# Performance work log

Hardware: AMD Instinct MI355X
Metric: run time of the kernel (lower is better)

The kernel has to match this reference:

```python
import jax, jax.numpy as jnp
import numpy as np

DIM, E, K, H = 1024, 8, 2, 4096

def setup_inputs() -> dict:
    key = jax.random.key(0)
    ks = jax.random.split(key, 5)
    s_in = 1.0 / np.sqrt(DIM)
    s_h = 1.0 / np.sqrt(H)
    return {
        "x": jax.random.normal(ks[0], (4, 2048, DIM), dtype=jnp.float32),
        "Wr": jax.random.normal(ks[1], (DIM, E), dtype=jnp.float32) * s_in,
        "W1": jax.random.normal(ks[2], (E, DIM, H), dtype=jnp.float32) * s_in,
        "b1": jnp.zeros((E, H), dtype=jnp.float32),
        "W2": jax.random.normal(ks[3], (E, H, DIM), dtype=jnp.float32) * s_h,
        "b2": jnp.zeros((E, DIM), dtype=jnp.float32),
    }

def reference(x, Wr, W1, b1, W2, b2):
    batch, seq, dim = x.shape
    x_flat = x.reshape(-1, dim)                      # [T, D]
    logits = x_flat @ Wr                             # [T, E]
    w, ind = jax.lax.top_k(logits, K)                # [T, K]
    w = jax.nn.softmax(w, axis=-1)
    # combine[t, e] = sum_i w[t, i] * (ind[t, i] == e)
    combine = jnp.einsum('tke,tk->te', jax.nn.one_hot(ind, E, dtype=x.dtype), w)  # [T, E]

    def body(acc, params):
        W1e, b1e, W2e, b2e, ce = params
        h = jax.nn.gelu(x_flat @ W1e + b1e, approximate=False)  # exact GELU (torch nn.GELU default)
        y = h @ W2e + b2e                                        # [T, D]
        return acc + ce[:, None] * y, None

    out0 = jnp.zeros_like(x_flat)
    out, _ = jax.lax.scan(body, out0, (W1, b1, W2, b2, combine.T))
    return out.reshape(batch, seq, dim)
```

## Files before the change

### kernel.cpp

```cpp
#include <hip/hip_runtime.h>
#include <hip/hip_bf16.h>

#define TDIM 1024
#define NEXP 8
#define NHID 4096

typedef __hip_bfloat16 bf16;
typedef __attribute__((ext_vector_type(8))) short bf16x8;
typedef __attribute__((ext_vector_type(8))) unsigned short u16x8;
typedef __attribute__((ext_vector_type(4))) float f32x4;

__device__ __forceinline__ void gload_lds16(void* lds, const void* g) {
  __builtin_amdgcn_global_load_lds(
      (const __attribute__((address_space(1))) unsigned int*)g,
      (__attribute__((address_space(3))) unsigned int*)lds, 16, 0, 0);
}

__device__ __forceinline__ unsigned short f2bf_bits(float f) {
  __hip_bfloat16 b = __float2bfloat16(f);
  unsigned short u;
  __builtin_memcpy(&u, &b, 2);
  return u;
}

__device__ __forceinline__ float bf2f(unsigned short u) {
  union { unsigned int i; float f; } c;
  c.i = ((unsigned int)u) << 16;
  return c.f;
}

__device__ __forceinline__ void do_transpose(const float* __restrict__ src, bf16* __restrict__ dst,
                                             int R, int C, int bx, int by, int tid,
                                             float (*tile)[65]) {
  const int c0 = bx * 64, r0 = by * 64;
#pragma unroll
  for (int i = 0; i < 4; ++i) {
    int s = tid + i * 256;
    int r = s >> 4, cg = (s & 15) * 4;
    float4 v = *reinterpret_cast<const float4*>(src + (size_t)(r0 + r) * C + c0 + cg);
    tile[r][cg] = v.x;
    tile[r][cg + 1] = v.y;
    tile[r][cg + 2] = v.z;
    tile[r][cg + 3] = v.w;
  }
  __syncthreads();
#pragma unroll
  for (int i = 0; i < 2; ++i) {
    int s = tid + i * 256;
    int c = s >> 3, rg = (s & 7) * 8;
    u16x8 o;
#pragma unroll
    for (int j = 0; j < 8; ++j) o[j] = f2bf_bits(tile[rg + j][c]);
    *reinterpret_cast<u16x8*>(dst + (size_t)(c0 + c) * R + r0 + rg) = o;
  }
}

__global__ __launch_bounds__(256) void prep_kernel(
    const float* __restrict__ W1, bf16* __restrict__ W1T, const float* __restrict__ W2,
    bf16* __restrict__ W2T, const float* __restrict__ x, bf16* __restrict__ xb,
    const float* __restrict__ Wr, int* __restrict__ idx, float* __restrict__ wtok,
    int* __restrict__ cnt, int T) {
  __shared__ float tile[64][65];
  const int pb = blockIdx.x;
  const int tid = threadIdx.x;
  if (pb < 8192) {
    const int bx = pb & 63, by = (pb >> 6) & 15, e = pb >> 10;
    do_transpose(W1 + (size_t)e * TDIM * NHID, W1T + (size_t)e * TDIM * NHID, TDIM, NHID, bx, by,
                 tid, tile);
  } else if (pb < 16384) {
    const int p = pb - 8192;
    const int bx = p & 15, by = (p >> 4) & 63, e = p >> 10;
    do_transpose(W2 + (size_t)e * TDIM * NHID, W2T + (size_t)e * TDIM * NHID, NHID, TDIM, bx, by,
                 tid, tile);
  } else {
    const int p = pb - 16384;
    const int wave = p * 4 + (tid >> 6);
    const int lane = tid & 63;
    if (wave >= T) return;
    const float4* xr4 = reinterpret_cast<const float4*>(x + (size_t)wave * TDIM);
    bf16* xbrow = xb + (size_t)wave * TDIM;
    float acc[NEXP];
#pragma unroll
    for (int e = 0; e < NEXP; ++e) acc[e] = 0.f;
    const float4* wr4 = reinterpret_cast<const float4*>(Wr);
#pragma unroll
    for (int i = 0; i < TDIM / 256; ++i) {
      float4 xv = xr4[lane + i * 64];
      ushort4 o;
      o.x = f2bf_bits(xv.x);
      o.y = f2bf_bits(xv.y);
      o.z = f2bf_bits(xv.z);
      o.w = f2bf_bits(xv.w);
      *reinterpret_cast<ushort4*>(xbrow + (lane + i * 64) * 4) = o;
      int row = (lane + i * 64) * 4;
#pragma unroll
      for (int j = 0; j < 4; ++j) {
        float xs = (&xv.x)[j];
        float4 wa = wr4[(row + j) * 2];
        float4 wb = wr4[(row + j) * 2 + 1];
        acc[0] += xs * wa.x;
        acc[1] += xs * wa.y;
        acc[2] += xs * wa.z;
        acc[3] += xs * wa.w;
        acc[4] += xs * wb.x;
        acc[5] += xs * wb.y;
        acc[6] += xs * wb.z;
        acc[7] += xs * wb.w;
      }
    }
#pragma unroll
    for (int e = 0; e < NEXP; ++e) {
      float v = acc[e];
#pragma unroll
      for (int s = 32; s; s >>= 1) v += __shfl_xor(v, s);
      acc[e] = v;
    }
    if (lane == 0) {
      int e0 = 0;
      float l0 = acc[0];
      for (int e = 1; e < NEXP; ++e)
        if (acc[e] > l0) { l0 = acc[e]; e0 = e; }
      int e1 = -1;
      float l1 = -INFINITY;
      for (int e = 0; e < NEXP; ++e)
        if (e != e0 && acc[e] > l1) { l1 = acc[e]; e1 = e; }
      float z = __expf(l1 - l0);
      idx[wave * 2] = e0;
      idx[wave * 2 + 1] = e1;
      wtok[wave * 2] = 1.f / (1.f + z);
      wtok[wave * 2 + 1] = z / (1.f + z);
      atomicAdd(&cnt[e0], 1);
      atomicAdd(&cnt[e1], 1);
    }
  }
}

__global__ void scan_kernel(const int* __restrict__ cnt, int* __restrict__ offs) {
  if (threadIdx.x == 0 && blockIdx.x == 0) {
    int s = 0;
    for (int e = 0; e < NEXP; ++e) { offs[e] = s; s += cnt[e]; }
  }
}

__global__ void build_perm_kernel(const int* __restrict__ idx, const int* __restrict__ offs,
                                  int* __restrict__ fill, int* __restrict__ perm,
                                  int* __restrict__ islot, int T) {
  int t = blockIdx.x * blockDim.x + threadIdx.x;
  if (t >= T) return;
#pragma unroll
  for (int k = 0; k < 2; ++k) {
    int e = idx[t * 2 + k];
    int p = offs[e] + atomicAdd(&fill[e], 1);
    perm[p] = t;
    islot[t * 2 + k] = p;
  }
}

template <int KD, int ND, bool GATHER, bool GELU>
__global__ __launch_bounds__(512, 2) void moe_gemm8(
    const bf16* __restrict__ A, const bf16* __restrict__ BT, const float* __restrict__ bias,
    const int* __restrict__ perm, const int* __restrict__ cnt, const int* __restrict__ offs,
    bf16* __restrict__ Dst, int nm, int nn) {
  __shared__ short lds[65536];

  const int nwg = NEXP * nm * nn;
  const int bid = blockIdx.x;
  const int wg = (bid & 7) * (nwg >> 3) + (bid >> 3);
  const int e = wg / (nm * nn);
  const int rem = wg % (nm * nn);
  const int mb = rem / nn, nb = rem % nn;

  const int ce = cnt[e];
  const int m0 = mb * 256;
  if (m0 >= ce) return;
  const int base = offs[e];
  const int n0 = nb * 256;
  const int tid = threadIdx.x;
  const int lane = tid & 63;
  const int wid = tid >> 6;
  const int wm = wid >> 2, wn = wid & 3;
  const int lcol = lane & 15;
  const int lkg = (lane >> 4) * 8;

  const int kxs0 = ((lkg << 1) ^ ((lcol & 7) << 4)) >> 1;
  const int kxs1 = (((lkg + 32) << 1) ^ ((lcol & 7) << 4)) >> 1;
  int aRow[4], bRow[2];
#pragma unroll
  for (int mm = 0; mm < 4; ++mm) aRow[mm] = (wm * 64 + mm * 16 + lcol) << 6;
#pragma unroll
  for (int n2 = 0; n2 < 2; ++n2) bRow[n2] = (wn * 32 + n2 * 16 + lcol) << 6;

  const bf16* aP[2][2];
  const bf16* bP[2][2];
#pragma unroll
  for (int h = 0; h < 2; ++h)
#pragma unroll
    for (int i = 0; i < 2; ++i) {
      int s = tid + i * 512;
      int srow = s >> 3;
      int kof = ((s & 7) ^ (srow & 7)) * 8;
      int grow = m0 + h * 128 + srow;
      if (grow > ce - 1) grow = ce - 1;
      size_t arow = GATHER ? (size_t)perm[base + grow] : (size_t)(base + grow);
      aP[h][i] = A + arow * KD + kof;
      bP[h][i] = BT + ((size_t)e * ND + n0 + h * 128 + srow) * KD + kof;
    }

  f32x4 acc[8][4];
#pragma unroll
  for (int m = 0; m < 8; ++m)
#pragma unroll
    for (int n = 0; n < 4; ++n) acc[m][n] = (f32x4){0.f, 0.f, 0.f, 0.f};

  bf16x8 fA[4][2], fB[2][2];

#define STAGE(SBUF, OP, HF, kof)                                                     \
  {                                                                                  \
    char* sd = (char*)lds + (SBUF) * 65536 + (OP) * 32768 + (HF) * 16384 + tid * 16; \
    gload_lds16(sd, ((OP) ? bP[HF][0] : aP[HF][0]) + (kof));                         \
    gload_lds16(sd + 8192, ((OP) ? bP[HF][1] : aP[HF][1]) + (kof));                  \
  }

#define PHASE(QM, QN, RA, RB, SOP, SHF, SBUF, CBUF, kof, DO_VM)                      \
  {                                                                                  \
    STAGE(SBUF, SOP, SHF, kof);                                                      \
    if (DO_VM) asm volatile("s_waitcnt vmcnt(6)" ::: "memory");                      \
    __builtin_amdgcn_s_barrier();                                                    \
    asm volatile("" ::: "memory");                                                   \
    if (RA) {                                                                        \
      const short* Ab = lds + (CBUF) * 32768 + (QM) * 8192;                          \
      _Pragma("unroll") for (int mm = 0; mm < 4; ++mm) {                             \
        fA[mm][0] = *(const bf16x8*)(Ab + aRow[mm] + kxs0);                          \
        fA[mm][1] = *(const bf16x8*)(Ab + aRow[mm] + kxs1);                          \
      }                                                                              \
    }                                                                                \
    if (RB) {                                                                        \
      const short* Bb = lds + (CBUF) * 32768 + 16384 + (QN) * 8192;                  \
      _Pragma("unroll") for (int n2 = 0; n2 < 2; ++n2) {                             \
        fB[n2][0] = *(const bf16x8*)(Bb + bRow[n2] + kxs0);                          \
        fB[n2][1] = *(const bf16x8*)(Bb + bRow[n2] + kxs1);                          \
      }                                                                              \
    }                                                                                \
    asm volatile("s_waitcnt lgkmcnt(0)" ::: "memory");                               \
    __builtin_amdgcn_s_setprio(1);                                                   \
    _Pragma("unroll") for (int mm = 0; mm < 4; ++mm)                                 \
        _Pragma("unroll") for (int n2 = 0; n2 < 2; ++n2) {                           \
      acc[(QM) * 4 + mm][(QN) * 2 + n2] = __builtin_amdgcn_mfma_f32_16x16x32_bf16(   \
          fA[mm][0], fB[n2][0], acc[(QM) * 4 + mm][(QN) * 2 + n2], 0, 0, 0);         \
      acc[(QM) * 4 + mm][(QN) * 2 + n2] = __builtin_amdgcn_mfma_f32_16x16x32_bf16(   \
          fA[mm][1], fB[n2][1], acc[(QM) * 4 + mm][(QN) * 2 + n2], 0, 0, 0);         \
    }                                                                                \
    __builtin_amdgcn_s_setprio(0);                                                   \
  }

  STAGE(0, 0, 0, 0);
  STAGE(0, 1, 0, 0);
  STAGE(0, 0, 1, 0);
  STAGE(0, 1, 1, 0);

  const int NI = KD / 128;
  for (int itv = 0; itv < NI; ++itv) {
    const int k1 = itv * 128 + 64;
    int k2 = itv * 128 + 128;
    if (k2 >= KD) k2 = 0;
    PHASE(0, 0, 1, 1, 0, 0, 1, 0, k1, 1)
    PHASE(1, 0, 1, 0, 1, 0, 1, 0, k1, 1)
    PHASE(1, 1, 0, 1, 0, 1, 1, 0, k1, 1)
    PHASE(0, 1, 1, 0, 1, 1, 1, 0, k1, 0)
    PHASE(0, 0, 1, 1, 0, 0, 0, 1, k2, 1)
    PHASE(1, 0, 1, 0, 1, 0, 0, 1, k2, 1)
    PHASE(1, 1, 0, 1, 0, 1, 0, 1, k2, 1)
    PHASE(0, 1, 1, 0, 1, 1, 0, 1, k2, 0)
  }
#undef PHASE
#undef STAGE

  float bv[4];
#pragma unroll
  for (int ni = 0; ni < 4; ++ni)
    bv[ni] = bias[e * ND + n0 + (ni >> 1) * 128 + wn * 32 + (ni & 1) * 16 + lcol];
  const int lr4 = (lane >> 4) * 4;
#pragma unroll
  for (int mi = 0; mi < 8; ++mi) {
    const int rbase = m0 + (mi >> 2) * 128 + wm * 64 + (mi & 3) * 16 + lr4;
#pragma unroll
    for (int r = 0; r < 4; ++r) {
      int grow = rbase + r;
      if (grow < ce) {
        bf16* drow = Dst + (size_t)(base + grow) * ND;
#pragma unroll
        for (int ni = 0; ni < 4; ++ni) {
          int col = n0 + (ni >> 1) * 128 + wn * 32 + (ni & 1) * 16 + lcol;
          float v = acc[mi][ni][r] + bv[ni];
          if (GELU) v = 0.5f * v * (1.0f + erff(v * 0.70710678118654752f));
          drow[col] = __float2bfloat16(v);
        }
      }
    }
  }
}

__global__ void combine_kernel(const bf16* __restrict__ y, const int* __restrict__ islot,
                               const float* __restrict__ wtok, float* __restrict__ out) {
  const int t = blockIdx.x;
  const int d = threadIdx.x * 4;
  const int s0 = islot[t * 2], s1 = islot[t * 2 + 1];
  const float w0 = wtok[t * 2], w1 = wtok[t * 2 + 1];
  ushort4 ya = *reinterpret_cast<const ushort4*>(y + (size_t)s0 * TDIM + d);
  ushort4 yb = *reinterpret_cast<const ushort4*>(y + (size_t)s1 * TDIM + d);
  float4 o;
  o.x = w0 * bf2f(ya.x) + w1 * bf2f(yb.x);
  o.y = w0 * bf2f(ya.y) + w1 * bf2f(yb.y);
  o.z = w0 * bf2f(ya.z) + w1 * bf2f(yb.z);
  o.w = w0 * bf2f(ya.w) + w1 * bf2f(yb.w);
  *reinterpret_cast<float4*>(out + (size_t)t * TDIM + d) = o;
}

extern "C" void kernel_launch(void* const* d_in, const int* in_sizes, int n_in, void* d_out,
                              int out_size, void* d_ws, size_t ws_size, hipStream_t stream) {
  const float* x = (const float*)d_in[0];
  const float* Wr = (const float*)d_in[1];
  const float* W1 = (const float*)d_in[2];
  const float* b1 = (const float*)d_in[3];
  const float* W2 = (const float*)d_in[4];
  const float* b2 = (const float*)d_in[5];
  float* out = (float*)d_out;
  const int T = in_sizes[0] / TDIM;

  size_t off = 0;
  auto alloc = [&](size_t bytes) {
    void* q = (char*)d_ws + off;
    off += (bytes + 255) & ~(size_t)255;
    return q;
  };
  bf16* xb = (bf16*)alloc((size_t)T * TDIM * 2);
  bf16* W1T = (bf16*)alloc((size_t)NEXP * TDIM * NHID * 2);
  bf16* W2T = (bf16*)alloc((size_t)NEXP * TDIM * NHID * 2);
  bf16* h = (bf16*)alloc((size_t)2 * T * NHID * 2);
  int* idx = (int*)alloc((size_t)T * 2 * 4);
  float* wtok = (float*)alloc((size_t)T * 2 * 4);
  int* perm = (int*)alloc((size_t)T * 2 * 4);
  int* islot = (int*)alloc((size_t)T * 2 * 4);
  int* cnt = (int*)alloc(256);
  int* fill = cnt + 8;
  int* offs = cnt + 16;
  bf16* y = W1T;

  hipMemsetAsync(cnt, 0, 64, stream);

  prep_kernel<<<18432, 256, 0, stream>>>(W1, W1T, W2, W2T, x, xb, Wr, idx, wtok, cnt, T);
  scan_kernel<<<1, 64, 0, stream>>>(cnt, offs);
  build_perm_kernel<<<(T + 255) / 256, 256, 0, stream>>>(idx, offs, fill, perm, islot, T);

  moe_gemm8<TDIM, NHID, true, true><<<NEXP * 32 * 16, 512, 0, stream>>>(
      xb, W1T, b1, perm, cnt, offs, h, 32, 16);
  moe_gemm8<NHID, TDIM, false, false><<<NEXP * 32 * 4, 512, 0, stream>>>(
      h, W2T, b2, perm, cnt, offs, y, 32, 4);

  combine_kernel<<<T, 256, 0, stream>>>(y, islot, wtok, out);
}
```

Baseline: 782.6 us.

## Replace weight transpose with k-chunked bf16 layout read directly by GEMM

The LDS-tiled fp32->bf16 transpose of W1/W2 is replaced by a per-thread conversion into a [K/8][N][8] chunked layout, where each output vector gathers 8 strided rows. The GEMM B-operand addressing is changed to load 16-byte chunks from this layout, so the transpose's shared-memory round trip and barrier go away and fewer prep blocks are launched. The strided per-element reads in the conversion are coalesced across threads along N, but the change also alters B-load access patterns in the GEMM, where consecutive rows now sit in adjacent 16-byte chunks.

New measurement: 794.4 us. Within noise of the previous version (+1.5%).

```diff
diff --git a/kernel.cpp b/kernel.cpp
--- a/kernel.cpp
+++ b/kernel.cpp
@@ -29,51 +29,32 @@
   return c.f;
 }
 
-__device__ __forceinline__ void do_transpose(const float* __restrict__ src, bf16* __restrict__ dst,
-                                             int R, int C, int bx, int by, int tid,
-                                             float (*tile)[65]) {
-  const int c0 = bx * 64, r0 = by * 64;
-#pragma unroll
-  for (int i = 0; i < 4; ++i) {
-    int s = tid + i * 256;
-    int r = s >> 4, cg = (s & 15) * 4;
-    float4 v = *reinterpret_cast<const float4*>(src + (size_t)(r0 + r) * C + c0 + cg);
-    tile[r][cg] = v.x;
-    tile[r][cg + 1] = v.y;
-    tile[r][cg + 2] = v.z;
-    tile[r][cg + 3] = v.w;
-  }
-  __syncthreads();
-#pragma unroll
-  for (int i = 0; i < 2; ++i) {
-    int s = tid + i * 256;
-    int c = s >> 3, rg = (s & 7) * 8;
-    u16x8 o;
-#pragma unroll
-    for (int j = 0; j < 8; ++j) o[j] = f2bf_bits(tile[rg + j][c]);
-    *reinterpret_cast<u16x8*>(dst + (size_t)(c0 + c) * R + r0 + rg) = o;
-  }
+__device__ __forceinline__ void cvt_chunk(const float* __restrict__ src, bf16* __restrict__ dst,
+                                          int c, int kqShift, int nMask, int rowLen) {
+  const int kq = c >> kqShift;
+  const int n = c & nMask;
+  const float* s = src + ((size_t)kq * 8) * rowLen + n;
+  u16x8 o;
+#pragma unroll
+  for (int j = 0; j < 8; ++j) o[j] = f2bf_bits(s[(size_t)j * rowLen]);
+  *reinterpret_cast<u16x8*>(dst + (size_t)c * 8) = o;
 }
 
 __global__ __launch_bounds__(256) void prep_kernel(
-    const float* __restrict__ W1, bf16* __restrict__ W1T, const float* __restrict__ W2,
-    bf16* __restrict__ W2T, const float* __restrict__ x, bf16* __restrict__ xb,
+    const float* __restrict__ W1, bf16* __restrict__ W1C, const float* __restrict__ W2,
+    bf16* __restrict__ W2C, const float* __restrict__ x, bf16* __restrict__ xb,
     const float* __restrict__ Wr, int* __restrict__ idx, float* __restrict__ wtok,
     int* __restrict__ cnt, int T) {
-  __shared__ float tile[64][65];
   const int pb = blockIdx.x;
   const int tid = threadIdx.x;
   if (pb < 8192) {
-    const int bx = pb & 63, by = (pb >> 6) & 15, e = pb >> 10;
-    do_transpose(W1 + (size_t)e * TDIM * NHID, W1T + (size_t)e * TDIM * NHID, TDIM, NHID, bx, by,
-                 tid, tile);
-  } else if (pb < 16384) {
+    const int id = pb * 256 + tid;
+    cvt_chunk(W1, W1C, id, 12, 4095, 4096);
+    cvt_chunk(W1, W1C, id + (1 << 21), 12, 4095, 4096);
+    cvt_chunk(W2, W2C, id, 10, 1023, 1024);
+    cvt_chunk(W2, W2C, id + (1 << 21), 10, 1023, 1024);
+  } else {
     const int p = pb - 8192;
-    const int bx = p & 15, by = (p >> 4) & 63, e = p >> 10;
-    do_transpose(W2 + (size_t)e * TDIM * NHID, W2T + (size_t)e * TDIM * NHID, NHID, TDIM, bx, by,
-                 tid, tile);
-  } else {
-    const int p = pb - 16384;
     const int wave = p * 4 + (tid >> 6);
     const int lane = tid & 63;
     if (wave >= T) return;
@@ -158,7 +139,7 @@
 
 template <int KD, int ND, bool GATHER, bool GELU>
 __global__ __launch_bounds__(512, 2) void moe_gemm8(
-    const bf16* __restrict__ A, const bf16* __restrict__ BT, const float* __restrict__ bias,
+    const bf16* __restrict__ A, const bf16* __restrict__ BC, const float* __restrict__ bias,
     const int* __restrict__ perm, const int* __restrict__ cnt, const int* __restrict__ offs,
     bf16* __restrict__ Dst, int nm, int nn) {
   __shared__ short lds[65536];
@@ -198,12 +179,12 @@
     for (int i = 0; i < 2; ++i) {
       int s = tid + i * 512;
       int srow = s >> 3;
-      int kof = ((s & 7) ^ (srow & 7)) * 8;
+      int ksrc = (s & 7) ^ (srow & 7);
       int grow = m0 + h * 128 + srow;
       if (grow > ce - 1) grow = ce - 1;
       size_t arow = GATHER ? (size_t)perm[base + grow] : (size_t)(base + grow);
-      aP[h][i] = A + arow * KD + kof;
-      bP[h][i] = BT + ((size_t)e * ND + n0 + h * 128 + srow) * KD + kof;
+      aP[h][i] = A + arow * KD + ksrc * 8;
+      bP[h][i] = BC + (size_t)e * KD * ND + ((size_t)ksrc * ND + (n0 + h * 128 + srow)) * 8;
     }
 
   f32x4 acc[8][4];
@@ -214,16 +195,21 @@
 
   bf16x8 fA[4][2], fB[2][2];
 
-#define STAGE(SBUF, OP, HF, kof)                                                     \
+#define STAGE(SBUF, OP, HF, kA, kB)                                                  \
   {                                                                                  \
     char* sd = (char*)lds + (SBUF) * 65536 + (OP) * 32768 + (HF) * 16384 + tid * 16; \
-    gload_lds16(sd, ((OP) ? bP[HF][0] : aP[HF][0]) + (kof));                         \
-    gload_lds16(sd + 8192, ((OP) ? bP[HF][1] : aP[HF][1]) + (kof));                  \
-  }
-
-#define PHASE(QM, QN, RA, RB, SOP, SHF, SBUF, CBUF, kof, DO_VM)                      \
+    if (OP) {                                                                        \
+      gload_lds16(sd, bP[HF][0] + (kB));                                             \
+      gload_lds16(sd + 8192, bP[HF][1] + (kB));                                      \
+    } else {                                                                         \
+      gload_lds16(sd, aP[HF][0] + (kA));                                             \
+      gload_lds16(sd + 8192, aP[HF][1] + (kA));                                      \
+    }                                                                                \
+  }
+
+#define PHASE(QM, QN, RA, RB, SOP, SHF, SBUF, CBUF, kA, kB, DO_VM)                   \
   {                                                                                  \
-    STAGE(SBUF, SOP, SHF, kof);                                                      \
+    STAGE(SBUF, SOP, SHF, kA, kB);                                                   \
     if (DO_VM) asm volatile("s_waitcnt vmcnt(6)" ::: "memory");                      \
     __builtin_amdgcn_s_barrier();                                                    \
     asm volatile("" ::: "memory");                                                   \
@@ -253,24 +239,25 @@
     __builtin_amdgcn_s_setprio(0);                                                   \
   }
 
-  STAGE(0, 0, 0, 0);
-  STAGE(0, 1, 0, 0);
-  STAGE(0, 0, 1, 0);
-  STAGE(0, 1, 1, 0);
+  STAGE(0, 0, 0, 0, 0);
+  STAGE(0, 1, 0, 0, 0);
+  STAGE(0, 0, 1, 0, 0);
+  STAGE(0, 1, 1, 0, 0);
 
   const int NI = KD / 128;
   for (int itv = 0; itv < NI; ++itv) {
     const int k1 = itv * 128 + 64;
     int k2 = itv * 128 + 128;
     if (k2 >= KD) k2 = 0;
-    PHASE(0, 0, 1, 1, 0, 0, 1, 0, k1, 1)
-    PHASE(1, 0, 1, 0, 1, 0, 1, 0, k1, 1)
-    PHASE(1, 1, 0, 1, 0, 1, 1, 0, k1, 1)
-    PHASE(0, 1, 1, 0, 1, 1, 1, 0, k1, 0)
-    PHASE(0, 0, 1, 1, 0, 0, 0, 1, k2, 1)
-    PHASE(1, 0, 1, 0, 1, 0, 0, 1, k2, 1)
-    PHASE(1, 1, 0, 1, 0, 1, 0, 1, k2, 1)
-    PHASE(0, 1, 1, 0, 1, 1, 0, 1, k2, 0)
+    const int k1B = k1 * ND, k2B = k2 * ND;
+    PHASE(0, 0, 1, 1, 0, 0, 1, 0, k1, k1B, 1)
+    PHASE(1, 0, 1, 0, 1, 0, 1, 0, k1, k1B, 1)
+    PHASE(1, 1, 0, 1, 0, 1, 1, 0, k1, k1B, 1)
+    PHASE(0, 1, 1, 0, 1, 1, 1, 0, k1, k1B, 0)
+    PHASE(0, 0, 1, 1, 0, 0, 0, 1, k2, k2B, 1)
+    PHASE(1, 0, 1, 0, 1, 0, 0, 1, k2, k2B, 1)
+    PHASE(1, 1, 0, 1, 0, 1, 0, 1, k2, k2B, 1)
+    PHASE(0, 1, 1, 0, 1, 1, 0, 1, k2, k2B, 0)
   }
 #undef PHASE
 #undef STAGE
@@ -334,8 +321,8 @@
     return q;
   };
   bf16* xb = (bf16*)alloc((size_t)T * TDIM * 2);
-  bf16* W1T = (bf16*)alloc((size_t)NEXP * TDIM * NHID * 2);
-  bf16* W2T = (bf16*)alloc((size_t)NEXP * TDIM * NHID * 2);
+  bf16* W1C = (bf16*)alloc((size_t)NEXP * TDIM * NHID * 2);
+  bf16* W2C = (bf16*)alloc((size_t)NEXP * TDIM * NHID * 2);
   bf16* h = (bf16*)alloc((size_t)2 * T * NHID * 2);
   int* idx = (int*)alloc((size_t)T * 2 * 4);
   float* wtok = (float*)alloc((size_t)T * 2 * 4);
@@ -344,18 +331,18 @@
   int* cnt = (int*)alloc(256);
   int* fill = cnt + 8;
   int* offs = cnt + 16;
-  bf16* y = W1T;
+  bf16* y = W1C;
 
   hipMemsetAsync(cnt, 0, 64, stream);
 
-  prep_kernel<<<18432, 256, 0, stream>>>(W1, W1T, W2, W2T, x, xb, Wr, idx, wtok, cnt, T);
+  prep_kernel<<<10240, 256, 0, stream>>>(W1, W1C, W2, W2C, x, xb, Wr, idx, wtok, cnt, T);
   scan_kernel<<<1, 64, 0, stream>>>(cnt, offs);
   build_perm_kernel<<<(T + 255) / 256, 256, 0, stream>>>(idx, offs, fill, perm, islot, T);
 
   moe_gemm8<TDIM, NHID, true, true><<<NEXP * 32 * 16, 512, 0, stream>>>(
-      xb, W1T, b1, perm, cnt, offs, h, 32, 16);
+      xb, W1C, b1, perm, cnt, offs, h, 32, 16);
   moe_gemm8<NHID, TDIM, false, false><<<NEXP * 32 * 4, 512, 0, stream>>>(
-      h, W2T, b2, perm, cnt, offs, y, 32, 4);
+      h, W2C, b2, perm, cnt, offs, y, 32, 4);
 
   combine_kernel<<<T, 256, 0, stream>>>(y, islot, wtok, out);
 }
```
